# Kernel tuning notes

Hardware: AMD Instinct MI355X
Metric: run time of the kernel (lower is better)

## Reference

```python
import jax, jax.numpy as jnp
from jax import lax
import numpy as np

B, C, H, W = 4, 64, 256, 256
OUT = 64


def setup_inputs() -> dict:
    key = jax.random.key(0)
    k1, k2, k3 = jax.random.split(key, 3)
    x = jax.random.normal(k1, (B, C, H, W), dtype=jnp.float32)
    # kaiming-ish init; offset conv scaled small so sampled offsets stay moderate
    w_off = jax.random.normal(k2, (18, C, 3, 3), dtype=jnp.float32) * 0.05
    b_off = jnp.zeros((18,), dtype=jnp.float32)
    w_def = jax.random.normal(k3, (OUT, C, 3, 3), dtype=jnp.float32) * (2.0 / (9 * C)) ** 0.5
    b_def = jnp.zeros((OUT,), dtype=jnp.float32)
    return {"x": x, "w_off": w_off, "b_off": b_off, "w_def": w_def, "b_def": b_def}


def _bilinear_sample(img, ys, xs):
    """img: [B,C,H,W]; ys,xs: [B,H,W] float sample coords. Zero padding outside."""
    y0 = jnp.floor(ys)
    x0 = jnp.floor(xs)
    ly = ys - y0  # [B,H,W]
    lx = xs - x0
    y0i = y0.astype(jnp.int32)
    x0i = x0.astype(jnp.int32)

    def corner(yi, xi):
        valid = (yi >= 0) & (yi < H) & (xi >= 0) & (xi < W)
        yc = jnp.clip(yi, 0, H - 1)
        xc = jnp.clip(xi, 0, W - 1)
        # gather per batch: [C,H,W] indexed by [H,W],[H,W] -> [C,H,W]
        v = jax.vmap(lambda im, a, b: im[:, a, b])(img, yc, xc)  # [B,C,H,W]
        return v * valid[:, None, :, :].astype(img.dtype)

    v00 = corner(y0i, x0i)
    v01 = corner(y0i, x0i + 1)
    v10 = corner(y0i + 1, x0i)
    v11 = corner(y0i + 1, x0i + 1)
    ly = ly[:, None, :, :]
    lx = lx[:, None, :, :]
    return (v00 * (1 - ly) * (1 - lx) + v01 * (1 - ly) * lx
            + v10 * ly * (1 - lx) + v11 * ly * lx)


def reference(x, w_off, b_off, w_def, b_def):
    # offset conv: 3x3, stride 1, pad 1 ('SAME')
    offsets = lax.conv_general_dilated(x, w_off, (1, 1), 'SAME') + b_off[None, :, None, None]
    offsets = offsets.reshape(B, 9, 2, H, W)  # per-tap (dy, dx), torchvision ordering

    hh = jnp.arange(H, dtype=x.dtype)[None, :, None]  # [1,H,1]
    ww = jnp.arange(W, dtype=x.dtype)[None, None, :]  # [1,1,W]

    out = jnp.zeros((B, OUT, H, W), dtype=x.dtype)
    for k in range(9):  # fixed small kernel loop
        ki, kj = k // 3, k % 3
        ys = hh + (ki - 1) + offsets[:, k, 0]  # pad=1 -> base = h + ki - 1
        xs = ww + (kj - 1) + offsets[:, k, 1]
        sampled = _bilinear_sample(x, ys, xs)  # [B,C,H,W]
        out = out + jnp.einsum('bchw,oc->bohw', sampled, w_def[:, :, ki, kj])
    return out + b_def[None, :, None, None]
```

## Files before the change

kernel.cpp:

```cpp
#include <hip/hip_runtime.h>


typedef _Float16 half8 __attribute__((ext_vector_type(8)));
typedef _Float16 h2    __attribute__((ext_vector_type(2)));
typedef float floatx4  __attribute__((ext_vector_type(4)));

namespace {
constexpr int B_ = 4, C_ = 64, H_ = 256, W_ = 256, OUT_ = 64;
constexpr int HW_ = H_ * W_;
constexpr size_t XT_BYTES = (size_t)B_ * HW_ * C_ * 2;
constexpr size_t WOFF_OFF = XT_BYTES;
constexpr int    WOFF_N   = 9 * 2 * 2 * 64 * 8;
constexpr size_t WDEF_OFF = WOFF_OFF + (size_t)WOFF_N * 2;
constexpr int    WDEF_N   = 9 * 2 * 4 * 64 * 8;
}

__global__ __launch_bounds__(256)
void transpose_x(const float* __restrict__ x, _Float16* __restrict__ xt,
                 const float* __restrict__ w_off, const float* __restrict__ w_def,
                 _Float16* __restrict__ wof, _Float16* __restrict__ wdf)
{
    const int bid = blockIdx.x;
    const int b = bid >> 8, y = bid & 255;
    const int px = threadIdx.x;
    const float* __restrict__ xp = x + (size_t)b * C_ * HW_ + y * W_ + px;

    union { _Float16 h[64]; uint4 u[8]; } v;
#pragma unroll
    for (int c = 0; c < C_; ++c) v.h[c] = (_Float16)xp[(size_t)c * HW_];

    _Float16* __restrict__ d0 = xt + ((size_t)(bid * 8) * 256 + px) * 8;
#pragma unroll
    for (int k = 0; k < 8; ++k)
        *(uint4*)(d0 + (size_t)k * 256 * 8) = v.u[k];

    if (bid < 32) {
        const int i0 = bid * 256 + threadIdx.x;
        for (int s = i0; s < OUT_ * C_ * 9; s += 8192) {
            const int n = s / 576;
            const int r = s - n * 576;
            const int c = r / 9;
            const int tap = r - c * 9;
            const int idx = ((((tap * 2 + (c >> 5)) * 4 + (n >> 4)) * 64
                              + ((c >> 3) & 3) * 16 + (n & 15)) << 3) + (c & 7);
            wdf[idx] = (_Float16)w_def[s];
        }
        for (int s = i0; s < 18 * C_ * 9; s += 8192) {
            const int n = s / 576;
            const int r = s - n * 576;
            const int c = r / 9;
            const int tap = r - c * 9;
            const int idx = ((((tap * 2 + (c >> 5)) * 2 + (n >> 4)) * 64
                              + ((c >> 3) & 3) * 16 + (n & 15)) << 3) + (c & 7);
            wof[idx] = (_Float16)w_off[s];
        }
        for (int i = i0; i < WOFF_N; i += 8192) {
            const int lane = (i >> 3) & 63, nt = (i >> 9) & 1;
            if (nt == 1 && (lane & 15) >= 2) wof[i] = (_Float16)0.0f;
        }
    }
}

__device__ __forceinline__ void bilin_setup(float ys, float xs, int* a, float* w)
{
    const float y0f = floorf(ys), x0f = floorf(xs);
    const float ly = ys - y0f, lx = xs - x0f;
    const int y0 = (int)y0f, x0 = (int)x0f;
    const int y1 = y0 + 1, x1 = x0 + 1;
    const int y0c = min(max(y0, 0), H_ - 1);
    const int y1c = min(max(y1, 0), H_ - 1);
    const int x0c = min(max(x0, 0), W_ - 1);
    const int x1c = min(max(x1, 0), W_ - 1);
    const float fy0 = (y0 >= 0 && y0 < H_) ? 1.0f : 0.0f;
    const float fy1 = (y1 >= 0 && y1 < H_) ? 1.0f : 0.0f;
    const float fx0 = (x0 >= 0 && x0 < W_) ? 1.0f : 0.0f;
    const float fx1 = (x1 >= 0 && x1 < W_) ? 1.0f : 0.0f;
    a[0] = y0c * 2048 + x0c;  w[0] = (1.0f - ly) * (1.0f - lx) * fy0 * fx0;
    a[1] = y0c * 2048 + x1c;  w[1] = (1.0f - ly) * lx          * fy0 * fx1;
    a[2] = y1c * 2048 + x0c;  w[2] = ly          * (1.0f - lx) * fy1 * fx0;
    a[3] = y1c * 2048 + x1c;  w[3] = ly          * lx          * fy1 * fx1;
}

__global__ __launch_bounds__(256, 3)
void deform_main(const _Float16* __restrict__ xt,
                 const _Float16* __restrict__ wof,
                 const float* __restrict__ b_off,
                 const _Float16* __restrict__ wdf,
                 const float* __restrict__ b_def,
                 float* __restrict__ out)
{
    __shared__ float off_lds[128 * 18];

    const int tid = threadIdx.x;
    const int lane = tid & 63;
    const int wv = tid >> 6;
    const int lm = lane & 15;
    const int lq = lane >> 4;
    const int bid = blockIdx.x;
    const int uid = (bid & 7) * 256 + (bid >> 3);
    const int colc = uid & 7;
    const int rowg = (uid >> 3) & 63;
    const int b = uid >> 9;
    const int y0 = rowg * 4;
    const int y = y0 + wv;
    const int base = colc * 32;
    const _Float16* __restrict__ xtb = xt + (size_t)b * HW_ * C_;

    {
        floatx4 acc1[2][2];
#pragma unroll
        for (int pt = 0; pt < 2; ++pt)
#pragma unroll
            for (int nt = 0; nt < 2; ++nt) acc1[pt][nt] = (floatx4)0.0f;

        uint4 st1[2][2];
        bool  v1[2][2];

#define P1_ISSUE(TAP, KC, PAR) do {                                          \
        const int dy_ = (TAP) / 3 - 1, dx_ = (TAP) % 3 - 1;                  \
        const int ys_ = y + dy_;                                             \
        const bool yok_ = (unsigned)ys_ < 256u;                              \
        const int ysc_ = min(max(ys_, 0), 255);                              \
        _Pragma("unroll")                                                    \
        for (int pt_ = 0; pt_ < 2; ++pt_) {                                  \
            const int pxs_ = base + pt_ * 16 + lm + dx_;                     \
            v1[PAR][pt_] = yok_ && ((unsigned)pxs_ < 256u);                  \
            const int pxc_ = min(max(pxs_, 0), 255);                         \
            st1[PAR][pt_] = *(const uint4*)(xtb +                            \
                (size_t)(ysc_ * 2048 + ((KC) * 4 + lq) * 256 + pxc_) * 8);   \
        } } while (0)

        P1_ISSUE(0, 0, 0);
#pragma unroll
        for (int g = 0; g < 18; ++g) {
            const int tap = g >> 1, kc = g & 1, par = g & 1;
            if (g < 17) { P1_ISSUE((g + 1) >> 1, (g + 1) & 1, (g + 1) & 1); }
            half8 bfr[2];
#pragma unroll
            for (int nt = 0; nt < 2; ++nt)
                bfr[nt] = *(const half8*)(wof +
                    ((size_t)(((tap * 2 + kc) * 2 + nt) * 64 + lane)) * 8);
#pragma unroll
            for (int pt = 0; pt < 2; ++pt) {
                uint4 t = st1[par][pt];
                if (!v1[par][pt]) { t.x = 0u; t.y = 0u; t.z = 0u; t.w = 0u; }
                const half8 afr = __builtin_bit_cast(half8, t);
#pragma unroll
                for (int nt = 0; nt < 2; ++nt)
                    acc1[pt][nt] = __builtin_amdgcn_mfma_f32_16x16x32_f16(
                        afr, bfr[nt], acc1[pt][nt], 0, 0, 0);
            }
        }
#undef P1_ISSUE

#pragma unroll
        for (int nt = 0; nt < 2; ++nt) {
            const int j = nt * 16 + lm;
            if (j < 18) {
                const float bj = b_off[j];
#pragma unroll
                for (int pt = 0; pt < 2; ++pt) {
#pragma unroll
                    for (int r = 0; r < 4; ++r) {
                        const int lpx = wv * 32 + pt * 16 + lq * 4 + r;
                        off_lds[lpx * 18 + j] = acc1[pt][nt][r] + bj;
                    }
                }
            }
        }
    }
    __syncthreads();

    floatx4 acc[2][4];
#pragma unroll
    for (int pt = 0; pt < 2; ++pt)
#pragma unroll
        for (int ot = 0; ot < 4; ++ot) acc[pt][ot] = (floatx4)0.0f;

    int   ca2[2][2][4];
    h2    cw2[2][2][4];
    uint4 stc[2][2][4];

#define P2_BILIN(TAP, TP) do {                                               \
        const int ki_ = (TAP) / 3, kj_ = (TAP) % 3;                          \
        _Pragma("unroll")                                                    \
        for (int pt_ = 0; pt_ < 2; ++pt_) {                                  \
            const int lpx_ = wv * 32 + pt_ * 16 + lm;                        \
            const float2 o2_ = *(const float2*)&off_lds[lpx_ * 18 + (TAP) * 2]; \
            const float ys_ = (float)(y + ki_ - 1) + o2_.x;                  \
            const float xs_ = (float)(base + pt_ * 16 + lm + kj_ - 1) + o2_.y; \
            float cwf_[4];                                                   \
            bilin_setup(ys_, xs_, ca2[TP][pt_], cwf_);                       \
            _Pragma("unroll")                                                \
            for (int c_ = 0; c_ < 4; ++c_)                                   \
                cw2[TP][pt_][c_] = (h2)((_Float16)cwf_[c_]);                 \
        } } while (0)

#define P2_ISSUE(TP, KC, PAR) do {                                           \
        const int plane_ = ((KC) * 4 + lq) * 256;                            \
        _Pragma("unroll")                                                    \
        for (int pt_ = 0; pt_ < 2; ++pt_)                                    \
            _Pragma("unroll")                                                \
            for (int c_ = 0; c_ < 4; ++c_)                                   \
                stc[PAR][pt_][c_] = *(const uint4*)(xtb +                    \
                    (size_t)(ca2[TP][pt_][c_] + plane_) * 8);                \
        } while (0)

    P2_BILIN(0, 0);
    P2_ISSUE(0, 0, 0);

#pragma unroll
    for (int g = 0; g < 18; ++g) {
        const int tap = g >> 1, kc = g & 1, par = g & 1, tp = (g >> 1) & 1;

        if (kc == 0) {
            P2_ISSUE(tp, 1, 1);
        } else if (tap < 8) {
            P2_ISSUE(tp ^ 1, 0, 0);
        }

        half8 bfr[4];
#pragma unroll
        for (int ot = 0; ot < 4; ++ot)
            bfr[ot] = *(const half8*)(wdf +
                ((size_t)(((tap * 2 + kc) * 4 + ot) * 64 + lane)) * 8);

        if (kc == 0 && tap < 8) P2_BILIN(tap + 1, tp ^ 1);

#pragma unroll
        for (int pt = 0; pt < 2; ++pt) {
            union Uc { uint4 u; h2 p[4]; } cc0, cc1, cc2, cc3;
            cc0.u = stc[par][pt][0];
            cc1.u = stc[par][pt][1];
            cc2.u = stc[par][pt][2];
            cc3.u = stc[par][pt][3];
            union Rr { h2 s[4]; half8 v; } r;
#pragma unroll
            for (int k = 0; k < 4; ++k)
                r.s[k] = cw2[tp][pt][0] * cc0.p[k] + cw2[tp][pt][1] * cc1.p[k]
                       + cw2[tp][pt][2] * cc2.p[k] + cw2[tp][pt][3] * cc3.p[k];
#pragma unroll
            for (int ot = 0; ot < 4; ++ot)
                acc[pt][ot] = __builtin_amdgcn_mfma_f32_16x16x32_f16(
                    r.v, bfr[ot], acc[pt][ot], 0, 0, 0);
        }
    }
#undef P2_BILIN
#undef P2_ISSUE

#pragma unroll
    for (int ot = 0; ot < 4; ++ot) {
        const int o = ot * 16 + lm;
        const float bd = b_def[o];
#pragma unroll
        for (int pt = 0; pt < 2; ++pt) {
            const int pxs = base + pt * 16 + lq * 4;
            const floatx4 a = acc[pt][ot];
            float4 v = make_float4(a[0] + bd, a[1] + bd, a[2] + bd, a[3] + bd);
            *(float4*)&out[(((size_t)b * OUT_ + o) * H_ + y) * W_ + pxs] = v;
        }
    }
}

extern "C" void kernel_launch(void* const* d_in, const int* in_sizes, int n_in,
                              void* d_out, int out_size, void* d_ws, size_t ws_size,
                              hipStream_t stream)
{
    const float* x     = (const float*)d_in[0];
    const float* w_off = (const float*)d_in[1];
    const float* b_off = (const float*)d_in[2];
    const float* w_def = (const float*)d_in[3];
    const float* b_def = (const float*)d_in[4];
    float* out = (float*)d_out;

    _Float16* xt  = (_Float16*)d_ws;
    _Float16* wof = (_Float16*)((char*)d_ws + WOFF_OFF);
    _Float16* wdf = (_Float16*)((char*)d_ws + WDEF_OFF);

    transpose_x<<<dim3(B_ * H_), dim3(256), 0, stream>>>(
        x, xt, w_off, w_def, wof, wdf);
    deform_main<<<dim3(B_ * H_ * 2), dim3(256), 0, stream>>>(
        xt, wof, b_off, wdf, b_def, out);
}
```

Before: 224.8 us.

## Tile transpose through LDS, relax occupancy bound, pin load issue with sched barriers

The x transpose kernel now stages a half-row of all 64 channels in shared memory using float4 loads, then emits packed fp16 channel groups. This replaces the per-thread strided scalar loads, and the grid doubles to cover half-rows. The main kernel's launch bound drops from 3 to 2 waves per SIMD, giving the compiler more registers. Scheduling barriers after each prefetch issue keep the loads ahead of the MFMA work. The lower occupancy could hurt latency hiding, and the barriers constrain the compiler's instruction interleaving.

```diff
diff --git a/kernel.cpp b/kernel.cpp
--- a/kernel.cpp
+++ b/kernel.cpp
@@ -20,19 +20,33 @@
                  const float* __restrict__ w_off, const float* __restrict__ w_def,
                  _Float16* __restrict__ wof, _Float16* __restrict__ wdf)
 {
+    __shared__ float tile[64 * 132];
     const int bid = blockIdx.x;
-    const int b = bid >> 8, y = bid & 255;
-    const int px = threadIdx.x;
-    const float* __restrict__ xp = x + (size_t)b * C_ * HW_ + y * W_ + px;
-
-    union { _Float16 h[64]; uint4 u[8]; } v;
-#pragma unroll
-    for (int c = 0; c < C_; ++c) v.h[c] = (_Float16)xp[(size_t)c * HW_];
-
-    _Float16* __restrict__ d0 = xt + ((size_t)(bid * 8) * 256 + px) * 8;
-#pragma unroll
-    for (int k = 0; k < 8; ++k)
-        *(uint4*)(d0 + (size_t)k * 256 * 8) = v.u[k];
+    const int half = bid & 1;
+    const int row = bid >> 1;
+    const int b = row >> 8, y = row & 255;
+    const int t = threadIdx.x;
+    const float* __restrict__ xp = x + (size_t)b * C_ * HW_ + y * W_ + half * 128;
+
+#pragma unroll
+    for (int i = 0; i < 8; ++i) {
+        const int c = i * 8 + (t >> 5);
+        const int px = (t & 31) * 4;
+        const float4 v = *(const float4*)&xp[(size_t)c * HW_ + px];
+        *(float4*)&tile[c * 132 + px] = v;
+    }
+    __syncthreads();
+
+#pragma unroll
+    for (int rr = 0; rr < 4; ++rr) {
+        const int kcq = (t >> 7) * 4 + rr;
+        const int px = t & 127;
+        union { _Float16 h[8]; uint4 u; } g;
+#pragma unroll
+        for (int cc = 0; cc < 8; ++cc)
+            g.h[cc] = (_Float16)tile[(kcq * 8 + cc) * 132 + px];
+        *(uint4*)(xt + (((size_t)row * 8 + kcq) * 256 + half * 128 + px) * 8) = g.u;
+    }
 
     if (bid < 32) {
         const int i0 = bid * 256 + threadIdx.x;
@@ -81,7 +95,7 @@
     a[3] = y1c * 2048 + x1c;  w[3] = ly          * lx          * fy1 * fx1;
 }
 
-__global__ __launch_bounds__(256, 3)
+__global__ __launch_bounds__(256, 2)
 void deform_main(const _Float16* __restrict__ xt,
                  const _Float16* __restrict__ wof,
                  const float* __restrict__ b_off,
@@ -131,10 +145,14 @@
         } } while (0)
 
         P1_ISSUE(0, 0, 0);
+        __builtin_amdgcn_sched_barrier(0);
 #pragma unroll
         for (int g = 0; g < 18; ++g) {
             const int tap = g >> 1, kc = g & 1, par = g & 1;
-            if (g < 17) { P1_ISSUE((g + 1) >> 1, (g + 1) & 1, (g + 1) & 1); }
+            if (g < 17) {
+                P1_ISSUE((g + 1) >> 1, (g + 1) & 1, (g + 1) & 1);
+                __builtin_amdgcn_sched_barrier(0);
+            }
             half8 bfr[2];
 #pragma unroll
             for (int nt = 0; nt < 2; ++nt)
@@ -208,6 +226,7 @@
 
     P2_BILIN(0, 0);
     P2_ISSUE(0, 0, 0);
+    __builtin_amdgcn_sched_barrier(0);
 
 #pragma unroll
     for (int g = 0; g < 18; ++g) {
@@ -215,8 +234,10 @@
 
         if (kc == 0) {
             P2_ISSUE(tp, 1, 1);
+            __builtin_amdgcn_sched_barrier(0);
         } else if (tap < 8) {
             P2_ISSUE(tp ^ 1, 0, 0);
+            __builtin_amdgcn_sched_barrier(0);
         }
 
         half8 bfr[4];
@@ -277,7 +298,7 @@
     _Float16* wof = (_Float16*)((char*)d_ws + WOFF_OFF);
     _Float16* wdf = (_Float16*)((char*)d_ws + WDEF_OFF);
 
-    transpose_x<<<dim3(B_ * H_), dim3(256), 0, stream>>>(
+    transpose_x<<<dim3(B_ * H_ * 2), dim3(256), 0, stream>>>(
         x, xt, w_off, w_def, wof, wdf);
     deform_main<<<dim3(B_ * H_ * 2), dim3(256), 0, stream>>>(
         xt, wof, b_off, wdf, b_def, out);
```

Measured after the change: 223.5 us. About the same (-0.6%).
